# Optimization experiments

Measured on AMD Instinct MI355X. Metric: run time of the kernel, lower is better.

The kernel has to match this reference:

```python
import jax, jax.numpy as jnp
import numpy as np

SCALE = 0.25
POOL = (7, 7)
SR = 2          # sampling_ratio
EPS = 1e-5      # LayerNorm eps
B, N, C, H, W = 4, 256, 256, 128, 128
D = 1024
IN_DIM = C * POOL[0] * POOL[1]


def _layer_norm(x, g, b):
    m = x.mean(-1, keepdims=True)
    v = ((x - m) ** 2).mean(-1, keepdims=True)
    return (x - m) / jnp.sqrt(v + EPS) * g + b


def _roi_align_one(feat, ys, xs):
    # feat [C,H,W]; ys [N,PH]; xs [N,PW] sample coords in feature-map space
    Cc, Hh, Ww = feat.shape
    y = ys[:, :, None]                      # [N,PH,1]
    x = xs[:, None, :]                      # [N,1,PW]
    valid = (y > -1.0) & (y < Hh) & (x > -1.0) & (x < Ww)  # torchvision semantics
    yc = jnp.clip(y, 0.0, Hh - 1)
    xc = jnp.clip(x, 0.0, Ww - 1)
    y0 = jnp.floor(yc).astype(jnp.int32)
    x0 = jnp.floor(xc).astype(jnp.int32)
    y1 = jnp.minimum(y0 + 1, Hh - 1)
    x1 = jnp.minimum(x0 + 1, Ww - 1)
    ly = yc - y0; lx = xc - x0
    hy = 1.0 - ly; hx = 1.0 - lx
    flat = feat.reshape(Cc, Hh * Ww)
    g = lambda yi, xi: flat[:, yi * Ww + xi]            # [C,N,PH,PW]
    val = (hy * hx) * g(y0, x0) + (hy * lx) * g(y0, x1) \
        + (ly * hx) * g(y1, x0) + (ly * lx) * g(y1, x1)
    return jnp.where(valid, val, 0.0)                    # [C,N,PH,PW]


def roi_align(feats, boxes):
    # feats [B,C,H,W]; boxes [B,N,4] in image coords -> pooled [B,N,C,ph,pw]
    Bb, Cc, Hh, Ww = feats.shape
    ph, pw = POOL
    b = boxes * SCALE
    bx1, by1, bx2, by2 = b[..., 0], b[..., 1], b[..., 2], b[..., 3]
    rw = jnp.maximum(bx2 - bx1, 1.0)
    rh = jnp.maximum(by2 - by1, 1.0)
    bh = rh / ph
    bw = rw / pw
    # sample offset k -> bin k//SR, sub-sample k%SR: (k+0.5)/SR bin-units
    oy = (jnp.arange(ph * SR, dtype=feats.dtype) + 0.5) / SR
    ox = (jnp.arange(pw * SR, dtype=feats.dtype) + 0.5) / SR
    ys = by1[..., None] + bh[..., None] * oy             # [B,N,ph*SR]
    xs = bx1[..., None] + bw[..., None] * ox             # [B,N,pw*SR]
    vals = jax.vmap(_roi_align_one)(feats, ys, xs)       # [B,C,N,PH,PW]
    Nn = boxes.shape[1]
    vals = vals.transpose(0, 2, 1, 3, 4).reshape(Bb, Nn, Cc, ph, SR, pw, SR)
    return vals.mean(axis=(4, 6))                        # avg over 2x2 samples


def setup_inputs() -> dict:
    key = jax.random.key(0)
    ks = jax.random.split(key, 8)
    feats = jax.random.normal(ks[0], (B, C, H, W), dtype=jnp.float32)
    r = jax.random.uniform(ks[1], (B, N, 4), dtype=jnp.float32)
    x1 = r[..., 0] * (512 - 64)
    y1 = r[..., 1] * (512 - 64)
    x2 = x1 + 4.0 + r[..., 2] * 60.0
    y2 = y1 + 4.0 + r[..., 3] * 60.0
    lines_box = jnp.stack([x1, y1, x2, y2], axis=-1)
    img_sizes = jnp.full((B, 2), 512, dtype=jnp.int32)
    W1 = jax.random.normal(ks[2], (IN_DIM, D), dtype=jnp.float32) / np.sqrt(IN_DIM)
    b1 = jnp.zeros((D,), jnp.float32)
    W2 = jax.random.normal(ks[3], (D, D), dtype=jnp.float32) / np.sqrt(D)
    b2 = jnp.zeros((D,), jnp.float32)
    bbox_W = jax.random.normal(ks[4], (4, D), dtype=jnp.float32) / 2.0
    bbox_b = jnp.zeros((D,), jnp.float32)
    ln_bbox_g = jnp.ones((D,), jnp.float32); ln_bbox_b = jnp.zeros((D,), jnp.float32)
    ln_add_g = jnp.ones((D,), jnp.float32); ln_add_b = jnp.zeros((D,), jnp.float32)
    return {"feats": feats, "lines_box": lines_box, "img_sizes": img_sizes,
            "W1": W1, "b1": b1, "W2": W2, "b2": b2,
            "bbox_W": bbox_W, "bbox_b": bbox_b,
            "ln_bbox_g": ln_bbox_g, "ln_bbox_b": ln_bbox_b,
            "ln_add_g": ln_add_g, "ln_add_b": ln_add_b}


def reference(feats, lines_box, img_sizes, W1, b1, W2, b2, bbox_W, bbox_b,
              ln_bbox_g, ln_bbox_b, ln_add_g, ln_add_b):
    Bb = feats.shape[0]
    Hh, Ww = feats.shape[-2:]
    Nn = lines_box.shape[1]
    pooled = roi_align(feats, lines_box).reshape(Bb, Nn, -1)   # [B,N,C*ph*pw]
    h = jax.nn.relu(pooled @ W1 + b1) @ W2 + b2                # [B,N,D]
    # per-image box normalization: x*scale/feats_W, y*scale/feats_H
    norm = SCALE * jnp.array([1.0 / Ww, 1.0 / Hh, 1.0 / Ww, 1.0 / Hh], feats.dtype)
    nb = lines_box * norm
    p = _layer_norm(nb @ bbox_W + bbox_b, ln_bbox_g, ln_bbox_b)
    return _layer_norm(h + p, ln_add_g, ln_add_b)              # [B,N,D]
```

## Files before the change

### kernel.cpp

```cpp
#include <hip/hip_runtime.h>
#include <hip/hip_bf16.h>

typedef __attribute__((ext_vector_type(8))) short short8;
typedef __attribute__((ext_vector_type(4))) float floatx4;

#define AS1(p) ((const __attribute__((address_space(1))) void*)(p))
#define AS3(p) ((__attribute__((address_space(3))) void*)(p))

__device__ __forceinline__ float bf_lo(unsigned u) { return __uint_as_float(u << 16); }
__device__ __forceinline__ float bf_hi(unsigned u) { return __uint_as_float(u & 0xffff0000u); }

__global__ __launch_bounds__(256) void prep_kernel(
    const float* __restrict__ feats, const float* __restrict__ W1, const float* __restrict__ W2,
    __hip_bfloat16* __restrict__ featsT, __hip_bfloat16* __restrict__ W1T,
    __hip_bfloat16* __restrict__ W2T)
{
    __shared__ float tile[64][65];
    const int tx = threadIdx.x;
    const int ty = threadIdx.y;
    const int bid = blockIdx.x;

    const float* src;
    __hip_bfloat16* dst;
    size_t sstride, dstride;

    if (bid < 4096) {
        const int b  = bid >> 10;
        const int r  = bid & 1023;
        const int ct = r >> 8;
        const int ht = r & 255;
        src = feats  + ((size_t)(b * 256 + ct * 64)) * 16384 + ht * 64;
        sstride = 16384;
        dst = featsT + ((size_t)b * 16384 + ht * 64) * 256 + ct * 64;
        dstride = 256;
    } else if (bid < 7232) {
        int r = bid - 4096;
        const int bin = r / 64;
        r -= bin * 64;
        const int ct = r >> 4;
        const int nt = r & 15;
        src = W1  + ((size_t)(ct * 64) * 49 + bin) * 1024 + nt * 64;
        sstride = 49 * 1024;
        dst = W1T + (size_t)(nt * 64) * 12544 + bin * 256 + ct * 64;
        dstride = 12544;
    } else {
        int r = bid - 7232;
        const int rt = r >> 4, ct2 = r & 15;
        src = W2  + (size_t)(rt * 64) * 1024 + ct2 * 64;
        sstride = 1024;
        dst = W2T + (size_t)(ct2 * 64) * 1024 + rt * 64;
        dstride = 1024;
    }

    #pragma unroll
    for (int i = 0; i < 16; ++i)
        tile[ty + i * 4][tx] = src[(size_t)(ty + i * 4) * sstride + tx];
    __syncthreads();
    #pragma unroll
    for (int i = 0; i < 16; ++i)
        dst[(size_t)(ty + i * 4) * dstride + tx] = __float2bfloat16(tile[tx][ty + i * 4]);
}

__global__ __launch_bounds__(256) void roi_kernel4(
    const __hip_bfloat16* __restrict__ featsT, const float* __restrict__ boxes,
    __hip_bfloat16* __restrict__ pooled)
{
    __shared__ int   sy0[14], sy1[14], sx0[14], sx1[14];
    __shared__ float sly[14], svy[14], slx[14], svx[14];
    const int tid  = threadIdx.x;
    const int bn   = blockIdx.x >> 1;
    const int half = blockIdx.x & 1;
    if (tid < 28) {
        const int  i   = tid % 14;
        const bool isx = tid >= 14;
        const float lo = boxes[bn * 4 + (isx ? 0 : 1)] * 0.25f;
        const float hi = boxes[bn * 4 + (isx ? 2 : 3)] * 0.25f;
        const float szb = fmaxf(hi - lo, 1.0f) * (1.0f / 7.0f);
        const float coord = lo + szb * ((i + 0.5f) * 0.5f);
        const float valid = (coord > -1.0f && coord < 128.0f) ? 1.0f : 0.0f;
        const float cc = fminf(fmaxf(coord, 0.0f), 127.0f);
        const int i0 = (int)floorf(cc);
        const int i1 = min(i0 + 1, 127);
        const float l = cc - (float)i0;
        if (isx) { sx0[i] = i0; sx1[i] = i1; slx[i] = l; svx[i] = valid; }
        else     { sy0[i] = i0; sy1[i] = i1; sly[i] = l; svy[i] = valid; }
    }
    __syncthreads();
    const int wave = tid >> 6;
    const int lane = tid & 63;
    const int sub  = lane >> 5;
    const int co   = lane & 31;
    const int b    = bn >> 8;
    const __hip_bfloat16* fb = featsT + (size_t)b * 4194304 + co * 8;
    __hip_bfloat16* po = pooled + (size_t)bn * 12544 + co * 8;

    const int pstart = (half ? 12 : 0) + wave;
    const int pend   = half ? 25 : 12;
    for (int p = pstart; p < pend; p += 4) {
        int bin = 2 * p + sub;
        if (bin > 48) bin = 48;
        const int ph = (bin * 37) >> 8;
        const int pw = bin - ph * 7;
        float s0 = 0.f, s1 = 0.f, s2 = 0.f, s3 = 0.f;
        float s4 = 0.f, s5 = 0.f, s6 = 0.f, s7 = 0.f;
        #pragma unroll
        for (int sy = 0; sy < 2; ++sy) {
            const int iy = ph * 2 + sy;
            const int y0 = sy0[iy], y1 = sy1[iy];
            const float ly = sly[iy], wy = svy[iy];
            const float hy = 1.f - ly;
            #pragma unroll
            for (int sx = 0; sx < 2; ++sx) {
                const int ix = pw * 2 + sx;
                const int x0 = sx0[ix], x1 = sx1[ix];
                const float lx = slx[ix], wx = svx[ix];
                const float hx = 1.f - lx;
                const uint4 u00 = *(const uint4*)(fb + (((y0 << 7) + x0) * 256));
                const uint4 u01 = *(const uint4*)(fb + (((y0 << 7) + x1) * 256));
                const uint4 u10 = *(const uint4*)(fb + (((y1 << 7) + x0) * 256));
                const uint4 u11 = *(const uint4*)(fb + (((y1 << 7) + x1) * 256));
                const float wv  = wy * wx;
                const float w00 = hy * hx * wv, w01 = hy * lx * wv;
                const float w10 = ly * hx * wv, w11 = ly * lx * wv;
                s0 += w00 * bf_lo(u00.x) + w01 * bf_lo(u01.x) + w10 * bf_lo(u10.x) + w11 * bf_lo(u11.x);
                s1 += w00 * bf_hi(u00.x) + w01 * bf_hi(u01.x) + w10 * bf_hi(u10.x) + w11 * bf_hi(u11.x);
                s2 += w00 * bf_lo(u00.y) + w01 * bf_lo(u01.y) + w10 * bf_lo(u10.y) + w11 * bf_lo(u11.y);
                s3 += w00 * bf_hi(u00.y) + w01 * bf_hi(u01.y) + w10 * bf_hi(u10.y) + w11 * bf_hi(u11.y);
                s4 += w00 * bf_lo(u00.z) + w01 * bf_lo(u01.z) + w10 * bf_lo(u10.z) + w11 * bf_lo(u11.z);
                s5 += w00 * bf_hi(u00.z) + w01 * bf_hi(u01.z) + w10 * bf_hi(u10.z) + w11 * bf_hi(u11.z);
                s6 += w00 * bf_lo(u00.w) + w01 * bf_lo(u01.w) + w10 * bf_lo(u10.w) + w11 * bf_lo(u11.w);
                s7 += w00 * bf_hi(u00.w) + w01 * bf_hi(u01.w) + w10 * bf_hi(u10.w) + w11 * bf_hi(u11.w);
            }
        }
        union { __hip_bfloat16 h[8]; uint4 u; } o;
        o.h[0] = __float2bfloat16(s0 * 0.25f);
        o.h[1] = __float2bfloat16(s1 * 0.25f);
        o.h[2] = __float2bfloat16(s2 * 0.25f);
        o.h[3] = __float2bfloat16(s3 * 0.25f);
        o.h[4] = __float2bfloat16(s4 * 0.25f);
        o.h[5] = __float2bfloat16(s5 * 0.25f);
        o.h[6] = __float2bfloat16(s6 * 0.25f);
        o.h[7] = __float2bfloat16(s7 * 0.25f);
        *(uint4*)(po + bin * 256) = o.u;
    }
}

__global__ __launch_bounds__(512, 2) void gemm1_8phase(
    const __hip_bfloat16* __restrict__ A,
    const __hip_bfloat16* __restrict__ BT,
    __hip_bfloat16* __restrict__ Cpart)
{
    constexpr int K = 12544;
    constexpr int KCHUNK = 896;
    constexpr int NKT = 14;
    constexpr int ITERS = 7;

    __shared__ char lds[131072];

    const int bid = blockIdx.x;
    const int xcd = bid & 7;
    const int sl  = bid >> 3;
    const int z   = xcd + 8 * (sl >> 4);
    if (z >= 14) return;
    const int tile = sl & 15;
    const int by = tile >> 2, bx = tile & 3;
    const int m0 = by << 8, n0 = bx << 8;
    const int k0 = z * KCHUNK;

    const int tid  = threadIdx.x;
    const int lane = tid & 63;
    const int wave = tid >> 6;
    const int wm   = wave >> 2;
    const int wn   = wave & 3;
    const int l15  = lane & 15;
    const int kq   = (lane >> 4) << 3;

    floatx4 acc[8][4] = {};
    short8 bf[4][2];

    auto stage = [&](const __hip_bfloat16* gsrc, int ldsoff) {
        #pragma unroll
        for (int j = 0; j < 2; ++j) {
            const int lin = j * 8192 + tid * 16;
            const int r   = lin >> 7;
            const int cs  = ((lin & 127) ^ ((r & 7) << 4)) >> 1;
            __builtin_amdgcn_global_load_lds(AS1(gsrc + (size_t)r * K + cs),
                                             AS3(lds + ldsoff + lin), 16, 0, 0);
        }
    };

#define PHASE(SLOT, MQ, FIRSTB, STAGE_STMT, VM)                                    \
    {                                                                               \
        if (FIRSTB) {                                                               \
            _Pragma("unroll")                                                       \
            for (int nf = 0; nf < 4; ++nf) {                                        \
                const int nl = wn * 64 + nf * 16 + l15;                             \
                const int bh = nl >> 7, br = nl & 127;                              \
                _Pragma("unroll")                                                   \
                for (int ks = 0; ks < 2; ++ks)                                      \
                    bf[nf][ks] = *(const short8*)(lds + (SLOT) * 65536 + 32768      \
                        + bh * 16384 + br * 128                                     \
                        + (((ks * 32 + kq) * 2) ^ ((br & 7) << 4)));                \
            }                                                                       \
        }                                                                           \
        short8 af[2][2];                                                            \
        _Pragma("unroll")                                                           \
        for (int mf = 0; mf < 2; ++mf) {                                            \
            const int ar = (MQ) * 32 + mf * 16 + l15;                               \
            _Pragma("unroll")                                                       \
            for (int ks = 0; ks < 2; ++ks)                                          \
                af[mf][ks] = *(const short8*)(lds + (SLOT) * 65536 + wm * 16384     \
                    + ar * 128 + (((ks * 32 + kq) * 2) ^ ((ar & 7) << 4)));         \
        }                                                                           \
        STAGE_STMT;                                                                 \
        __builtin_amdgcn_s_barrier();                                               \
        asm volatile("s_waitcnt lgkmcnt(0)" ::: "memory");                          \
        __builtin_amdgcn_s_setprio(1);                                              \
        _Pragma("unroll")                                                           \
        for (int mf = 0; mf < 2; ++mf)                                              \
            _Pragma("unroll")                                                       \
            for (int nf = 0; nf < 4; ++nf)                                          \
                _Pragma("unroll")                                                   \
                for (int ks = 0; ks < 2; ++ks)                                      \
                    acc[(MQ) * 2 + mf][nf] = __builtin_amdgcn_mfma_f32_16x16x32_bf16( \
                        af[mf][ks], bf[nf][ks], acc[(MQ) * 2 + mf][nf], 0, 0, 0);   \
        __builtin_amdgcn_s_setprio(0);                                              \
        if (VM) asm volatile("s_waitcnt vmcnt(4)" ::: "memory");                    \
        __builtin_amdgcn_s_barrier();                                               \
    }

    stage(BT + (size_t)n0 * K + k0,               32768);
    stage(BT + (size_t)(n0 + 128) * K + k0,       32768 + 16384);
    stage(A  + (size_t)m0 * K + k0,               0);
    stage(A  + (size_t)(m0 + 128) * K + k0,       16384);
    stage(BT + (size_t)n0 * K + k0 + 64,          65536 + 32768);
    stage(BT + (size_t)(n0 + 128) * K + k0 + 64,  65536 + 32768 + 16384);
    asm volatile("s_waitcnt vmcnt(4)" ::: "memory");
    __builtin_amdgcn_s_barrier();

    for (int it = 0; it < ITERS; ++it) {
        const int t1 = 2 * it + 1;
        int t2 = 2 * it + 2; if (t2 > NKT - 1) t2 = NKT - 1;
        int t3 = 2 * it + 3; if (t3 > NKT - 1) t3 = NKT - 1;
        PHASE(0, 0, true,  stage(A  + (size_t)m0 * K + k0 + t1 * 64,          65536),          0);
        PHASE(0, 1, false, stage(A  + (size_t)(m0 + 128) * K + k0 + t1 * 64,  65536 + 16384),  0);
        PHASE(0, 2, false, stage(BT + (size_t)n0 * K + k0 + t2 * 64,          32768),          0);
        PHASE(0, 3, false, stage(BT + (size_t)(n0 + 128) * K + k0 + t2 * 64,  32768 + 16384),  1);
        PHASE(1, 0, true,  stage(A  + (size_t)m0 * K + k0 + t2 * 64,          0),              0);
        PHASE(1, 1, false, stage(A  + (size_t)(m0 + 128) * K + k0 + t2 * 64,  16384),          0);
        PHASE(1, 2, false, stage(BT + (size_t)n0 * K + k0 + t3 * 64,          65536 + 32768),  0);
        PHASE(1, 3, false, stage(BT + (size_t)(n0 + 128) * K + k0 + t3 * 64,  65536 + 32768 + 16384), 1);
    }
#undef PHASE

    __hip_bfloat16* cp = Cpart + (size_t)z * (1024 * 1024) + (size_t)m0 * 1024 + n0;
    const int r4 = (lane >> 4) << 2;
    #pragma unroll
    for (int mi = 0; mi < 8; ++mi)
        #pragma unroll
        for (int nf = 0; nf < 4; ++nf)
            #pragma unroll
            for (int r = 0; r < 4; ++r)
                cp[(size_t)(wm * 128 + mi * 16 + r4 + r) * 1024 + wn * 64 + nf * 16 + l15] =
                    __float2bfloat16(acc[mi][nf][r]);
}

__global__ __launch_bounds__(256) void gemm_bf16_kernel(
    const __hip_bfloat16* __restrict__ A,
    const __hip_bfloat16* __restrict__ BT,
    __hip_bfloat16* __restrict__ Cpart,
    int Mdim, int Ndim, int K, int kChunk)
{
    __shared__ __hip_bfloat16 lsA[128 * 64];
    __shared__ __hip_bfloat16 lsB[128 * 64];
    const int tid  = threadIdx.x;
    const int lane = tid & 63;
    const int wave = tid >> 6;
    const int wrow = (wave >> 1) << 6;
    const int wcol = (wave & 1) << 6;
    const int m0 = blockIdx.y << 7;
    const int n0 = blockIdx.x << 7;
    const int k0 = blockIdx.z * kChunk;

    floatx4 acc[4][4] = {};

    const int strow = tid >> 3;
    const int scol  = ((tid & 7) ^ (strow & 7)) << 3;
    const __hip_bfloat16* aSrc = A  + (size_t)(m0 + strow) * K + k0 + scol;
    const __hip_bfloat16* bSrc = BT + (size_t)(n0 + strow) * K + k0 + scol;
    __hip_bfloat16* ldsA = lsA + tid * 8;
    __hip_bfloat16* ldsB = lsB + tid * 8;
    const size_t rowJump = (size_t)32 * K;

    const int row16 = lane & 15;
    const int kg    = (lane >> 4) << 3;
    const int nk = kChunk >> 6;
    for (int kk = 0; kk < nk; ++kk) {
        __syncthreads();
        #pragma unroll
        for (int g = 0; g < 4; ++g) {
            __builtin_amdgcn_global_load_lds(AS1(aSrc + g * rowJump), AS3(ldsA + g * 2048), 16, 0, 0);
            __builtin_amdgcn_global_load_lds(AS1(bSrc + g * rowJump), AS3(ldsB + g * 2048), 16, 0, 0);
        }
        __syncthreads();
        #pragma unroll
        for (int ks = 0; ks < 2; ++ks) {
            short8 af[4], bfr[4];
            #pragma unroll
            for (int m = 0; m < 4; ++m) {
                const int ar = wrow + m * 16 + row16;
                af[m] = *(const short8*)(lsA + ar * 64 + ((ks * 32 + kg) ^ ((ar & 7) << 3)));
            }
            #pragma unroll
            for (int n = 0; n < 4; ++n) {
                const int br = wcol + n * 16 + row16;
                bfr[n] = *(const short8*)(lsB + br * 64 + ((ks * 32 + kg) ^ ((br & 7) << 3)));
            }
            #pragma unroll
            for (int m = 0; m < 4; ++m)
                #pragma unroll
                for (int n = 0; n < 4; ++n)
                    acc[m][n] = __builtin_amdgcn_mfma_f32_16x16x32_bf16(af[m], bfr[n], acc[m][n], 0, 0, 0);
        }
        aSrc += 64; bSrc += 64;
    }
    __hip_bfloat16* cp = Cpart + (size_t)blockIdx.z * Mdim * Ndim + (size_t)m0 * Ndim + n0;
    const int r4 = (lane >> 4) << 2;
    #pragma unroll
    for (int m = 0; m < 4; ++m)
        #pragma unroll
        for (int n = 0; n < 4; ++n)
            #pragma unroll
            for (int r = 0; r < 4; ++r)
                cp[(size_t)(wrow + m * 16 + r4 + r) * Ndim + (wcol + n * 16 + row16)] =
                    __float2bfloat16(acc[m][n][r]);
}

__global__ __launch_bounds__(256) void reduce_relu_kernel(
    const __hip_bfloat16* __restrict__ part, const float* __restrict__ bias,
    __hip_bfloat16* __restrict__ out, int nsplit)
{
    const size_t MN = 1024 * 1024;
    const int idx = (blockIdx.x * 256 + threadIdx.x) * 8;
    float s[8] = {};
    for (int z = 0; z < nsplit; ++z) {
        const uint4 v = *(const uint4*)(part + z * MN + idx);
        s[0] += bf_lo(v.x); s[1] += bf_hi(v.x);
        s[2] += bf_lo(v.y); s[3] += bf_hi(v.y);
        s[4] += bf_lo(v.z); s[5] += bf_hi(v.z);
        s[6] += bf_lo(v.w); s[7] += bf_hi(v.w);
    }
    const int jb = idx & 1023;
    const floatx4 b0 = *(const floatx4*)(bias + jb);
    const floatx4 b1v = *(const floatx4*)(bias + jb + 4);
    union { __hip_bfloat16 h[8]; uint4 u; } o;
    #pragma unroll
    for (int i = 0; i < 4; ++i) {
        const float v0 = s[i] + b0[i];
        o.h[i] = __float2bfloat16(v0 > 0.0f ? v0 : 0.0f);
    }
    #pragma unroll
    for (int i = 0; i < 4; ++i) {
        const float v1 = s[4 + i] + b1v[i];
        o.h[4 + i] = __float2bfloat16(v1 > 0.0f ? v1 : 0.0f);
    }
    *(uint4*)(out + idx) = o.u;
}

__device__ inline void block_stats(float s, float ss, float* red, float& mean, float& rstd)
{
    #pragma unroll
    for (int o = 32; o > 0; o >>= 1) {
        s  += __shfl_down(s, o, 64);
        ss += __shfl_down(ss, o, 64);
    }
    const int wave = threadIdx.x >> 6;
    const int lane = threadIdx.x & 63;
    __syncthreads();
    if (lane == 0) { red[wave] = s; red[8 + wave] = ss; }
    __syncthreads();
    const float a = red[0] + red[1] + red[2] + red[3];
    const float b = red[8] + red[9] + red[10] + red[11];
    mean = a * (1.0f / 1024.0f);
    const float var = b * (1.0f / 1024.0f) - mean * mean;
    rstd = rsqrtf(var + 1e-5f);
}

__global__ __launch_bounds__(256) void final_kernel(
    const __hip_bfloat16* __restrict__ part2, const float* __restrict__ b2,
    const float* __restrict__ boxes,
    const float* __restrict__ bboxW, const float* __restrict__ bboxb,
    const float* __restrict__ g1, const float* __restrict__ bb1,
    const float* __restrict__ g2, const float* __restrict__ bb2,
    float* __restrict__ out)
{
    __shared__ float red[16];
    const int row = blockIdx.x;
    const int j0 = threadIdx.x * 4;
    const size_t MN = 1024 * 1024;

    floatx4 h = *(const floatx4*)(b2 + j0);
    #pragma unroll
    for (int z = 0; z < 4; ++z) {
        const uint2 v = *(const uint2*)(part2 + z * MN + (size_t)row * 1024 + j0);
        h[0] += bf_lo(v.x); h[1] += bf_hi(v.x);
        h[2] += bf_lo(v.y); h[3] += bf_hi(v.y);
    }

    const float sc = 0.25f / 128.0f;
    const float nb0 = boxes[row * 4 + 0] * sc;
    const float nb1 = boxes[row * 4 + 1] * sc;
    const float nb2 = boxes[row * 4 + 2] * sc;
    const float nb3 = boxes[row * 4 + 3] * sc;

    floatx4 p = *(const floatx4*)(bboxb + j0);
    p += nb0 * *(const floatx4*)(bboxW + j0);
    p += nb1 * *(const floatx4*)(bboxW + 1024 + j0);
    p += nb2 * *(const floatx4*)(bboxW + 2048 + j0);
    p += nb3 * *(const floatx4*)(bboxW + 3072 + j0);

    float mean, rstd;
    block_stats(p[0] + p[1] + p[2] + p[3],
                p[0]*p[0] + p[1]*p[1] + p[2]*p[2] + p[3]*p[3], red, mean, rstd);
    const floatx4 pg = *(const floatx4*)(g1 + j0);
    const floatx4 pb = *(const floatx4*)(bb1 + j0);
    floatx4 x;
    #pragma unroll
    for (int i = 0; i < 4; ++i)
        x[i] = h[i] + ((p[i] - mean) * rstd * pg[i] + pb[i]);

    block_stats(x[0] + x[1] + x[2] + x[3],
                x[0]*x[0] + x[1]*x[1] + x[2]*x[2] + x[3]*x[3], red, mean, rstd);
    const floatx4 og = *(const floatx4*)(g2 + j0);
    const floatx4 ob = *(const floatx4*)(bb2 + j0);
    floatx4 o;
    #pragma unroll
    for (int i = 0; i < 4; ++i)
        o[i] = (x[i] - mean) * rstd * og[i] + ob[i];
    *(floatx4*)(out + (size_t)row * 1024 + j0) = o;
}

extern "C" void kernel_launch(void* const* d_in, const int* in_sizes, int n_in,
                              void* d_out, int out_size, void* d_ws, size_t ws_size,
                              hipStream_t stream)
{
    const float* feats = (const float*)d_in[0];
    const float* boxes = (const float*)d_in[1];
    const float* W1    = (const float*)d_in[3];
    const float* b1    = (const float*)d_in[4];
    const float* W2    = (const float*)d_in[5];
    const float* b2    = (const float*)d_in[6];
    const float* bboxW = (const float*)d_in[7];
    const float* bboxb = (const float*)d_in[8];
    const float* g1    = (const float*)d_in[9];
    const float* bb1   = (const float*)d_in[10];
    const float* g2    = (const float*)d_in[11];
    const float* bb2   = (const float*)d_in[12];
    float* out = (float*)d_out;

    char* ws = (char*)d_ws;
    __hip_bfloat16* W1T    = (__hip_bfloat16*)(ws);
    __hip_bfloat16* W2T    = (__hip_bfloat16*)(ws + 25690112);
    __hip_bfloat16* pooled = (__hip_bfloat16*)(ws + 27787264);
    __hip_bfloat16* part1  = (__hip_bfloat16*)(ws + 53477376);
    __hip_bfloat16* part2  = part1;
    __hip_bfloat16* featsT = (__hip_bfloat16*)(ws + 53477376);
    __hip_bfloat16* A2     = (__hip_bfloat16*)(ws + 87031808);

    prep_kernel<<<7488, dim3(64, 4), 0, stream>>>(feats, W1, W2, featsT, W1T, W2T);
    roi_kernel4<<<2048, 256, 0, stream>>>(featsT, boxes, pooled);
    gemm1_8phase<<<256, 512, 0, stream>>>(pooled, W1T, part1);
    reduce_relu_kernel<<<512, 256, 0, stream>>>(part1, b1, A2, 14);
    gemm_bf16_kernel<<<dim3(8, 8, 4), 256, 0, stream>>>(A2, W2T, part2, 1024, 1024, 1024, 256);
    final_kernel<<<1024, 256, 0, stream>>>(part2, b2, boxes, bboxW, bboxb, g1, bb1, g2, bb2, out);
}
```

Baseline: 107.1 us.

## Widen prep transpose tiles with vectorized loads, 16-byte bf16 stores and swizzled LDS

```diff
diff --git a/kernel.cpp b/kernel.cpp
--- a/kernel.cpp
+++ b/kernel.cpp
@@ -10,55 +10,63 @@
 __device__ __forceinline__ float bf_lo(unsigned u) { return __uint_as_float(u << 16); }
 __device__ __forceinline__ float bf_hi(unsigned u) { return __uint_as_float(u & 0xffff0000u); }
 
-__global__ __launch_bounds__(256) void prep_kernel(
+__global__ __launch_bounds__(512) void prep_kernel(
     const float* __restrict__ feats, const float* __restrict__ W1, const float* __restrict__ W2,
     __hip_bfloat16* __restrict__ featsT, __hip_bfloat16* __restrict__ W1T,
     __hip_bfloat16* __restrict__ W2T)
 {
-    __shared__ float tile[64][65];
-    const int tx = threadIdx.x;
-    const int ty = threadIdx.y;
+    __shared__ float tile[256][68];
+    const int t = threadIdx.x;
+    const int w = t >> 6, l = t & 63;
     const int bid = blockIdx.x;
 
     const float* src;
     __hip_bfloat16* dst;
     size_t sstride, dstride;
 
-    if (bid < 4096) {
-        const int b  = bid >> 10;
-        const int r  = bid & 1023;
-        const int ct = r >> 8;
-        const int ht = r & 255;
-        src = feats  + ((size_t)(b * 256 + ct * 64)) * 16384 + ht * 64;
+    if (bid < 1024) {
+        const int b = bid >> 8, hwt = bid & 255;
+        src = feats + (size_t)b * 256 * 16384 + hwt * 64;
         sstride = 16384;
-        dst = featsT + ((size_t)b * 16384 + ht * 64) * 256 + ct * 64;
+        dst = featsT + ((size_t)b * 16384 + hwt * 64) * 256;
         dstride = 256;
-    } else if (bid < 7232) {
-        int r = bid - 4096;
-        const int bin = r / 64;
-        r -= bin * 64;
-        const int ct = r >> 4;
-        const int nt = r & 15;
-        src = W1  + ((size_t)(ct * 64) * 49 + bin) * 1024 + nt * 64;
+    } else if (bid < 1808) {
+        const int r = bid - 1024;
+        const int bin = r >> 4, nt = r & 15;
+        src = W1 + (size_t)bin * 1024 + nt * 64;
         sstride = 49 * 1024;
-        dst = W1T + (size_t)(nt * 64) * 12544 + bin * 256 + ct * 64;
+        dst = W1T + (size_t)(nt * 64) * 12544 + bin * 256;
         dstride = 12544;
     } else {
-        int r = bid - 7232;
-        const int rt = r >> 4, ct2 = r & 15;
-        src = W2  + (size_t)(rt * 64) * 1024 + ct2 * 64;
+        const int r = bid - 1808;
+        const int kt = r >> 4, nt = r & 15;
+        src = W2 + (size_t)(kt * 256) * 1024 + nt * 64;
         sstride = 1024;
-        dst = W2T + (size_t)(ct2 * 64) * 1024 + rt * 64;
+        dst = W2T + (size_t)(nt * 64) * 1024 + kt * 256;
         dstride = 1024;
     }
 
     #pragma unroll
-    for (int i = 0; i < 16; ++i)
-        tile[ty + i * 4][tx] = src[(size_t)(ty + i * 4) * sstride + tx];
+    for (int i = 0; i < 8; ++i) {
+        const int r  = i * 32 + w * 4 + (l >> 4);
+        const int c4 = (l & 15) * 4;
+        const float4 v = *(const float4*)(src + (size_t)r * sstride + c4);
+        *(float4*)&tile[r][c4 ^ (((r >> 3) & 15) << 2)] = v;
+    }
     __syncthreads();
-    #pragma unroll
-    for (int i = 0; i < 16; ++i)
-        dst[(size_t)(ty + i * 4) * dstride + tx] = __float2bfloat16(tile[tx][ty + i * 4]);
+
+    #pragma unroll
+    for (int i = 0; i < 4; ++i) {
+        const int d  = i * 16 + w * 2 + (l >> 5);
+        const int a  = l & 31;
+        const int c8 = a * 8;
+        const int dsw = d ^ ((a & 15) << 2);
+        union { __hip_bfloat16 h[8]; uint4 u; } o;
+        #pragma unroll
+        for (int j = 0; j < 8; ++j)
+            o.h[j] = __float2bfloat16(tile[c8 + j][dsw]);
+        *(uint4*)(dst + (size_t)d * dstride + c8) = o.u;
+    }
 }
 
 __global__ __launch_bounds__(256) void roi_kernel4(
@@ -467,7 +475,7 @@
     __hip_bfloat16* featsT = (__hip_bfloat16*)(ws + 53477376);
     __hip_bfloat16* A2     = (__hip_bfloat16*)(ws + 87031808);
 
-    prep_kernel<<<7488, dim3(64, 4), 0, stream>>>(feats, W1, W2, featsT, W1T, W2T);
+    prep_kernel<<<1872, 512, 0, stream>>>(feats, W1, W2, featsT, W1T, W2T);
     roi_kernel4<<<2048, 256, 0, stream>>>(featsT, boxes, pooled);
     gemm1_8phase<<<256, 512, 0, stream>>>(pooled, W1T, part1);
     reduce_relu_kernel<<<512, 256, 0, stream>>>(part1, b1, A2, 14);
```

After: 108.1 us. About the same (+0.9%).
